# Performance work log

Hardware: AMD Instinct MI355X
Metric: run time of the kernel (lower is better)

## Reference

```python
import jax, jax.numpy as jnp
import numpy as np
from jax import lax

C = 128; HEADS = 16; HD = 8; EPS = 1e-5

def _conv3x3(x, w):
    return lax.conv_general_dilated(x, w, (1, 1), 'SAME', dimension_numbers=('NCHW', 'OIHW', 'NCHW'))

def _cbr3(x, w, g, b):
    # Conv3x3 + BatchNorm(eval, running stats folded -> per-channel affine) + ReLU
    return jax.nn.relu(_conv3x3(x, w) * g[:, None, None] + b[:, None, None])

def _cbr1(x, w, g, b):
    y = jnp.einsum('bchw,oc->bohw', x, w)
    return jax.nn.relu(y * g[:, None, None] + b[:, None, None])

def _ln(t, g, b):
    mu = t.mean(-1, keepdims=True)
    va = ((t - mu) ** 2).mean(-1, keepdims=True)
    return (t - mu) / jnp.sqrt(va + EPS) * g + b

def _gconv1x1(xf, w, b, groups):
    # grouped 1x1 conv on flattened spatial dim: xf [B,Cin,N], w [Cout, Cin//groups]
    B, Cin, N = xf.shape
    Cout = w.shape[0]
    y = jnp.einsum('bgcn,goc->bgon', xf.reshape(B, groups, Cin // groups, N),
                   w.reshape(groups, Cout // groups, Cin // groups))
    return y.reshape(B, Cout, N) + b[:, None]

def _ss_softmax(a):
    # sign * sqrt(|a| + 1e-5) then softmax (GISSA's custom transform)
    a = jnp.sign(a) * jnp.sqrt(jnp.abs(a) + 1e-5)
    return jax.nn.softmax(a, axis=-1)

def _gissa(ximg, qkv_w, qkv_b, g, b, qkv2_w, qkv2_b):
    B, Cc, H, W = ximg.shape
    N = H * W
    xf = ximg.reshape(B, Cc, N)
    qkv = _gconv1x1(xf, qkv_w, qkv_b, HEADS).reshape(B, 3, HEADS, HD, N)
    q, k, v = qkv[:, 0], qkv[:, 1], qkv[:, 2]
    attn = _ss_softmax(jnp.einsum('bhdn,bhen->bhde', q, k) * HD ** -0.5)  # [B,h,hd,hd]
    x1 = jnp.einsum('bhde,bhen->bhdn', attn, v).reshape(B, Cc, N) + xf
    x1 = x1.reshape(B, HEADS, HD, N).transpose(0, 2, 1, 3).reshape(B, Cc, N)  # channel shuffle
    y = x1 * g[:, None] + b[:, None]  # BatchNorm eval affine
    xr = jax.nn.relu(y)
    qkv2 = _gconv1x1(xr, qkv2_w, qkv2_b, HD).reshape(B, 3, HD, HEADS, N)
    q2, k2, v2 = qkv2[:, 0], qkv2[:, 1], qkv2[:, 2]
    attn2 = _ss_softmax(jnp.einsum('bdhn,bdgn->bdhg', q2, k2) * HEADS ** -0.5)  # [B,hd,h,h]
    o = jnp.einsum('bdhg,bdgn->bdhn', attn2, v2).transpose(0, 2, 1, 3).reshape(B, Cc, N) + y
    return o.reshape(B, Cc, H, W)

def _swsa_calc(ximg, pi_w, pi_b, g, b, po_w, po_b):
    B, Cc, H, W = ximg.shape
    t = jnp.einsum('bcn,oc->bon', ximg.reshape(B, Cc, H * W), pi_w) + pi_b[:, None]
    t = t * g[:, None] + b[:, None]  # BN affine
    q = t[:, :Cc].transpose(0, 2, 1)  # [B,N,C]
    v = t[:, Cc:].transpose(0, 2, 1)
    atn = jax.nn.softmax(jnp.einsum('bnc,bmc->bnm', q, q) * Cc ** -0.5, axis=-1)
    y = jnp.einsum('bnm,bmc->bnc', atn, v).transpose(0, 2, 1)  # [B,C,N]
    y = (jnp.einsum('bcn,oc->bon', y, po_w) + po_b[:, None]).reshape(B, Cc, H, W)
    return y, atn

def _swsa_reuse(ximg, atn, pi_w, pi_b, g, b, po_w, po_b):
    B, Cc, H, W = ximg.shape
    t = jnp.einsum('bcn,oc->bon', ximg.reshape(B, Cc, H * W), pi_w) + pi_b[:, None]
    t = t * g[:, None] + b[:, None]
    v = t.transpose(0, 2, 1)
    y = (jnp.einsum('bnm,bmc->bnc', atn, v) * Cc ** -0.5).transpose(0, 2, 1)
    return (jnp.einsum('bcn,oc->bon', y, po_w) + po_b[:, None]).reshape(B, Cc, H, W)

def _forward(x, ssfe_w, ssfe_g, ssfe_b, cc_w, cc_g, cc_b, ln1_g, ln1_b, qkv_w, qkv_b, gbn_g, gbn_b, qkv2_w, qkv2_b, ln2_g, ln2_b, mlp_w1, mlp_b1, mlp_w2, mlp_b2, cs_w, cs_g, cs_b, lfe0_w, lfe0_g, lfe0_b, s0_pi_w, s0_pi_b, s0_bn_g, s0_bn_b, s0_po_w, s0_po_b, lfe1_w, lfe1_g, lfe1_b, s1_pi_w, s1_pi_b, s1_bn_g, s1_bn_b, s1_po_w, s1_po_b, lamuda, fc_w):
    B, Cin, H, W = x.shape
    N = H * W
    # SSFE stem (approximated as Conv3x3+BN+ReLU; source def unavailable)
    xs = _cbr3(x, ssfe_w, ssfe_g, ssfe_b)
    # channel branch: 1x1 CBR + SIT (LN -> GISSA -> residual -> LN -> MLP -> residual)
    xc = _cbr1(xs, cc_w, cc_g, cc_b)
    t = xc.reshape(B, C, N).transpose(0, 2, 1)  # [B,N,C]
    cur = _ln(t, ln1_g, ln1_b).transpose(0, 2, 1).reshape(B, C, H, W)
    t = t + _gissa(cur, qkv_w, qkv_b, gbn_g, gbn_b, qkv2_w, qkv2_b).reshape(B, C, N).transpose(0, 2, 1)
    h = _ln(t, ln2_g, ln2_b)
    h = jax.nn.gelu(h @ mlp_w1.T + mlp_b1, approximate=False) @ mlp_w2.T + mlp_b2
    t = t + h
    xc = t.transpose(0, 2, 1).reshape(B, C, H, W)
    # spatial branch: 3x3 CBR + SCA (LFE + SWSA with attention reuse)
    xp = _cbr3(xs, cs_w, cs_g, cs_b)
    xp = _cbr3(xp, lfe0_w, lfe0_g, lfe0_b) + xp
    y, atn = _swsa_calc(xp, s0_pi_w, s0_pi_b, s0_bn_g, s0_bn_b, s0_po_w, s0_po_b)
    xp = y + xp
    xp = _cbr3(xp, lfe1_w, lfe1_g, lfe1_b) + xp
    xp = _swsa_reuse(xp, atn, s1_pi_w, s1_pi_b, s1_bn_g, s1_bn_b, s1_po_w, s1_po_b) + xp
    lmd = jax.nn.sigmoid(lamuda[0])
    out = lmd * xc + (1.0 - lmd) * xp
    return out.mean(axis=(2, 3)) @ fc_w.T  # global avg pool + fc (dropout p=0 for HUST2013)

def setup_inputs():
    ks = iter(jax.random.split(jax.random.key(0), 64))
    def rn(shape, scale=0.05):
        return jax.random.normal(next(ks), shape, jnp.float32) * scale
    ones = lambda *s: jnp.ones(s, jnp.float32)
    zeros = lambda *s: jnp.zeros(s, jnp.float32)
    return dict(
        x=jax.random.normal(next(ks), (32, 144, 32, 32), jnp.float32),
        ssfe_w=rn((144, 144, 3, 3)), ssfe_g=ones(144), ssfe_b=zeros(144),
        cc_w=rn((128, 144)), cc_g=ones(128), cc_b=zeros(128),
        ln1_g=ones(128), ln1_b=zeros(128),
        qkv_w=rn((384, 8)), qkv_b=zeros(384),
        gbn_g=ones(128), gbn_b=zeros(128),
        qkv2_w=rn((384, 16)), qkv2_b=zeros(384),
        ln2_g=ones(128), ln2_b=zeros(128),
        mlp_w1=rn((512, 128)), mlp_b1=zeros(512),
        mlp_w2=rn((128, 512)), mlp_b2=zeros(128),
        cs_w=rn((128, 144, 3, 3)), cs_g=ones(128), cs_b=zeros(128),
        lfe0_w=rn((128, 128, 3, 3)), lfe0_g=ones(128), lfe0_b=zeros(128),
        s0_pi_w=rn((256, 128)), s0_pi_b=zeros(256), s0_bn_g=ones(256), s0_bn_b=zeros(256),
        s0_po_w=rn((128, 128)), s0_po_b=zeros(128),
        lfe1_w=rn((128, 128, 3, 3)), lfe1_g=ones(128), lfe1_b=zeros(128),
        s1_pi_w=rn((128, 128)), s1_pi_b=zeros(128), s1_bn_g=ones(128), s1_bn_b=zeros(128),
        s1_po_w=rn((128, 128)), s1_po_b=zeros(128),
        lamuda=jnp.full((1,), 0.5, jnp.float32),
        fc_w=rn((16, 128)),
    )

def reference(x, ssfe_w, ssfe_g, ssfe_b, cc_w, cc_g, cc_b, ln1_g, ln1_b, qkv_w, qkv_b, gbn_g, gbn_b, qkv2_w, qkv2_b, ln2_g, ln2_b, mlp_w1, mlp_b1, mlp_w2, mlp_b2, cs_w, cs_g, cs_b, lfe0_w, lfe0_g, lfe0_b, s0_pi_w, s0_pi_b, s0_bn_g, s0_bn_b, s0_po_w, s0_po_b, lfe1_w, lfe1_g, lfe1_b, s1_pi_w, s1_pi_b, s1_bn_g, s1_bn_b, s1_po_w, s1_po_b, lamuda, fc_w):
    return _forward(x, ssfe_w, ssfe_g, ssfe_b, cc_w, cc_g, cc_b, ln1_g, ln1_b, qkv_w, qkv_b, gbn_g, gbn_b, qkv2_w, qkv2_b, ln2_g, ln2_b, mlp_w1, mlp_b1, mlp_w2, mlp_b2, cs_w, cs_g, cs_b, lfe0_w, lfe0_g, lfe0_b, s0_pi_w, s0_pi_b, s0_bn_g, s0_bn_b, s0_po_w, s0_po_b, lfe1_w, lfe1_g, lfe1_b, s1_pi_w, s1_pi_b, s1_bn_g, s1_bn_b, s1_po_w, s1_po_b, lamuda, fc_w)
```

## Files before the change

### kernel.cpp

```cpp
#include <hip/hip_runtime.h>
#include <math.h>


static constexpr int NPIX = 1024;

typedef __attribute__((ext_vector_type(8))) short bf16x8;
typedef __attribute__((ext_vector_type(4))) float f32x4;
typedef __attribute__((ext_vector_type(8))) unsigned short u16x8;
typedef __attribute__((ext_vector_type(4))) unsigned short u16x4;

static __device__ __forceinline__ unsigned short f2bf(float f) {
    unsigned u = __builtin_bit_cast(unsigned, f);
    unsigned r = (u + 0x7fffu + ((u >> 16) & 1u)) >> 16;
    return (unsigned short)r;
}
static __device__ __forceinline__ float bf2f(unsigned short u) {
    unsigned v = ((unsigned)u) << 16;
    return __builtin_bit_cast(float, v);
}

__global__ __launch_bounds__(256) void prepack_convs(
    const float* __restrict__ ssfe_w, const float* __restrict__ cs_w,
    const float* __restrict__ lfe0_w, const float* __restrict__ lfe1_w,
    unsigned short* __restrict__ wssfe, unsigned short* __restrict__ wcs,
    unsigned short* __restrict__ wlfe0, unsigned short* __restrict__ wlfe1)
{
    int idx = blockIdx.x * 256 + threadIdx.x;
    const float* src;
    unsigned short* dst;
    int k, Cout, CIN, CINP;
    if (idx < 207360) {
        src = ssfe_w; dst = wssfe; k = idx; Cout = 144; CIN = 144; CINP = 160;
    } else if (idx < 391680) {
        src = cs_w; dst = wcs; k = idx - 207360; Cout = 128; CIN = 144; CINP = 160;
    } else if (idx < 539136) {
        src = lfe0_w; dst = wlfe0; k = idx - 391680; Cout = 128; CIN = 128; CINP = 128;
    } else if (idx < 686592) {
        src = lfe1_w; dst = wlfe1; k = idx - 539136; Cout = 128; CIN = 128; CINP = 128;
    } else return;
    int ci = k % CINP;
    int rem = k / CINP;
    int co = rem % Cout;
    int tap = rem / Cout;
    float v = (ci < CIN) ? src[((size_t)co * CIN + ci) * 9 + tap] : 0.f;
    dst[k] = f2bf(v);
}

__global__ __launch_bounds__(256) void prepack_lins(
    const float* __restrict__ cc_w, const float* __restrict__ pi0_w,
    const float* __restrict__ pi1_w, const float* __restrict__ po0_w,
    const float* __restrict__ po1_w, const float* __restrict__ w1,
    const float* __restrict__ w2, unsigned short* __restrict__ o)
{
    int idx = blockIdx.x * 256 + threadIdx.x;
    if (idx >= 233472) return;
    float v;
    if (idx < 20480) {
        int ci = idx % 160, co = idx / 160;
        v = (ci < 144) ? cc_w[co * 144 + ci] : 0.f;
    } else if (idx < 53248) {
        v = pi0_w[idx - 20480];
    } else if (idx < 69632) {
        v = pi1_w[idx - 53248];
    } else if (idx < 86016) {
        v = po0_w[idx - 69632];
    } else if (idx < 102400) {
        v = po1_w[idx - 86016];
    } else if (idx < 167936) {
        v = w1[idx - 102400];
    } else {
        v = w2[idx - 167936];
    }
    o[idx] = f2bf(v);
}

template <int CINP, int NCH, int M>
__global__ __launch_bounds__(256) void conv3x3_stg_kernel(
    const float* __restrict__ in, int CIN,
    const unsigned short* __restrict__ wrep,
    const float* __restrict__ g, const float* __restrict__ bb,
    unsigned short* __restrict__ outT, int Cout, int zcol)
{
    __shared__ unsigned short X[194 * 40];
    const int tid = threadIdx.x;
    const int b = blockIdx.x, gr = blockIdx.y, cg = blockIdx.z;
    const int co0 = cg * (M * 16);
    const int pbase = gr << 7;
    const int gbase = pbase - 33;
    const int wv = tid >> 6, lane = tid & 63;
    const int ll = lane & 15, lk = lane >> 4;
    const float* inb = in + ((size_t)b * CIN << 10);

    f32x4 acc[M][2];
#pragma unroll
    for (int i = 0; i < M; ++i)
#pragma unroll
        for (int j = 0; j < 2; ++j)
#pragma unroll
            for (int r = 0; r < 4; ++r) acc[i][j][r] = 0.f;

#pragma unroll 1
    for (int ch = 0; ch < NCH; ++ch) {
        const int c0 = ch << 5;
#pragma unroll 1
        for (int idx = tid; idx < 16 * 194; idx += 256) {
            const int ci2 = idx / 194;
            const int sp = idx - ci2 * 194;
            const int ci = c0 + ci2 * 2;
            const int gp = gbase + sp;
            const bool inr = (gp >= 0) & (gp < 1024);
            const float* p0 = inb + ((size_t)ci << 10);
            float a = (inr && ci < CIN) ? p0[gp] : 0.f;
            float c = (inr && (ci + 1) < CIN) ? p0[gp + 1024] : 0.f;
            *(unsigned*)&X[sp * 40 + ci2 * 2] =
                (unsigned)f2bf(a) | ((unsigned)f2bf(c) << 16);
        }
        __syncthreads();
#pragma unroll
        for (int tap = 0; tap < 9; ++tap) {
            const int soff = (tap / 3) * 32 + (tap % 3);
            const int dx = tap % 3;
            bf16x8 bfrag[2];
#pragma unroll
            for (int j = 0; j < 2; ++j) {
                const int p = wv * 32 + j * 16 + ll;
                bf16x8 v = *(const bf16x8*)&X[(p + soff) * 40 + lk * 8];
                const bool zed = (dx == 0 && j == 0 && ll == 0) ||
                                 (dx == 2 && j == 1 && ll == 15);
                if (zed) { bf16x8 z = {}; v = z; }
                bfrag[j] = v;
            }
            const unsigned short* wb =
                wrep + ((size_t)tap * Cout + co0) * CINP + c0 + lk * 8;
#pragma unroll
            for (int i = 0; i < M; ++i) {
                bf16x8 afr = *(const bf16x8*)(wb + (size_t)(i * 16 + ll) * CINP);
#pragma unroll
                for (int j = 0; j < 2; ++j)
                    acc[i][j] = __builtin_amdgcn_mfma_f32_16x16x32_bf16(
                        afr, bfrag[j], acc[i][j], 0, 0, 0);
            }
        }
        __syncthreads();
    }

#pragma unroll
    for (int i = 0; i < M; ++i) {
#pragma unroll
        for (int j = 0; j < 2; ++j) {
            const int px = pbase + wv * 32 + j * 16 + ll;
            u16x4 tp;
#pragma unroll
            for (int r = 0; r < 4; ++r) {
                const int co = co0 + i * 16 + lk * 4 + r;
                float v = fmaxf(acc[i][j][r] * g[co] + bb[co], 0.f);
                tp[r] = f2bf(v);
            }
            *(u16x4*)(outT + (((size_t)b << 10) + px) * CINP + co0 + i * 16 + lk * 4) = tp;
            if (cg == (int)gridDim.z - 1 && i == 0) {
                u16x4 z = {};
                *(u16x4*)(outT + (((size_t)b << 10) + px) * CINP + zcol + lk * 4) = z;
            }
        }
    }
}

template <int CINP>
__global__ __launch_bounds__(256) void conv3x3_lds_kernel(
    const unsigned short* __restrict__ xT,
    const unsigned short* __restrict__ wrep,
    const float* __restrict__ g, const float* __restrict__ bb,
    const unsigned short* __restrict__ resT,
    unsigned short* __restrict__ outT, int Cout)
{
    constexpr int PITCH = CINP + 8;
    constexpr int NCHK = CINP / 8;
    __shared__ unsigned short X[130 * PITCH];
    const int tid = threadIdx.x;
    const int b = blockIdx.x, gr = blockIdx.y;
    const int pbase = gr << 6;
    const int gbase = pbase - 33;
    const int wid = tid >> 6, lane = tid & 63;
    const int ll = lane & 15, lq = lane >> 4;
    const int co0w = wid << 5;
    const unsigned short* xb = xT + ((size_t)b << 10) * CINP;

#pragma unroll 1
    for (int idx = tid; idx < 130 * NCHK; idx += 256) {
        const int row = idx / NCHK;
        const int chunk = idx - row * NCHK;
        const int gp = gbase + row;
        u16x8 v = {};
        if (gp >= 0 && gp < 1024)
            v = *(const u16x8*)(xb + (size_t)gp * CINP + chunk * 8);
        *(u16x8*)&X[row * PITCH + chunk * 8] = v;
    }
    __syncthreads();

    f32x4 acc[2][4];
#pragma unroll
    for (int i = 0; i < 2; ++i)
#pragma unroll
        for (int j = 0; j < 4; ++j)
#pragma unroll
            for (int r = 0; r < 4; ++r) acc[i][j][r] = 0.f;

#pragma unroll
    for (int tap = 0; tap < 9; ++tap) {
        const int soff = (tap / 3) * 32 + (tap % 3);
        const int dx = tap % 3;
#pragma unroll
        for (int kc = 0; kc < CINP / 32; ++kc) {
            bf16x8 bfv[4];
#pragma unroll
            for (int j = 0; j < 4; ++j) {
                const int p = j * 16 + ll;
                bf16x8 v = *(const bf16x8*)&X[(p + soff) * PITCH + kc * 32 + lq * 8];
                const bool zed = (dx == 0 && (j & 1) == 0 && ll == 0) ||
                                 (dx == 2 && (j & 1) == 1 && ll == 15);
                if (zed) { bf16x8 z = {}; v = z; }
                bfv[j] = v;
            }
            const unsigned short* wb =
                wrep + ((size_t)tap * Cout + co0w) * CINP + kc * 32 + lq * 8;
#pragma unroll
            for (int i = 0; i < 2; ++i) {
                bf16x8 af = *(const bf16x8*)(wb + (size_t)(i * 16 + ll) * CINP);
#pragma unroll
                for (int j = 0; j < 4; ++j)
                    acc[i][j] = __builtin_amdgcn_mfma_f32_16x16x32_bf16(
                        af, bfv[j], acc[i][j], 0, 0, 0);
            }
        }
    }

#pragma unroll
    for (int i = 0; i < 2; ++i) {
        const int cob = co0w + i * 16 + lq * 4;
        float gv[4], bv[4];
#pragma unroll
        for (int r = 0; r < 4; ++r) { gv[r] = g[cob + r]; bv[r] = bb[cob + r]; }
#pragma unroll
        for (int j = 0; j < 4; ++j) {
            const int px = pbase + j * 16 + ll;
            const size_t rowT = ((size_t)((b << 10) + px)) << 7;
            u16x4 rv = {};
            if (resT) rv = *(const u16x4*)(resT + rowT + cob);
            u16x4 tp;
#pragma unroll
            for (int r = 0; r < 4; ++r) {
                float v = fmaxf(acc[i][j][r] * gv[r] + bv[r], 0.f);
                if (resT) v += bf2f(rv[r]);
                tp[r] = f2bf(v);
            }
            *(u16x4*)(outT + rowT + cob) = tp;
        }
    }
}

template <int KP>
__global__ __launch_bounds__(256) void lin_mfma_kernel(
    const unsigned short* __restrict__ xT, const unsigned short* __restrict__ wbf,
    const float* __restrict__ bias0, const float* __restrict__ g,
    const float* __restrict__ bb, const unsigned short* __restrict__ resT,
    float* __restrict__ outF, unsigned short* __restrict__ outBF,
    unsigned short* __restrict__ outT, int do_relu)
{
    const int tid = threadIdx.x;
    const int b = blockIdx.x;
    const int n0 = blockIdx.y << 6;
    const int wid = tid >> 6, lane = tid & 63;
    const int ll = lane & 15, lq = lane >> 4;
    const unsigned short* xb = xT + (size_t)((b << 10) + n0) * KP;

    f32x4 acc[2][4];
#pragma unroll
    for (int i = 0; i < 2; ++i)
#pragma unroll
        for (int j = 0; j < 4; ++j)
#pragma unroll
            for (int r = 0; r < 4; ++r) acc[i][j][r] = 0.f;

#pragma unroll
    for (int kk = 0; kk < KP / 32; ++kk) {
        bf16x8 af[2], bfv[4];
#pragma unroll
        for (int i = 0; i < 2; ++i)
            af[i] = *(const bf16x8*)(wbf + (size_t)(wid * 32 + i * 16 + ll) * KP + kk * 32 + lq * 8);
#pragma unroll
        for (int j = 0; j < 4; ++j)
            bfv[j] = *(const bf16x8*)(xb + (size_t)(j * 16 + ll) * KP + kk * 32 + lq * 8);
#pragma unroll
        for (int i = 0; i < 2; ++i)
#pragma unroll
            for (int j = 0; j < 4; ++j)
                acc[i][j] = __builtin_amdgcn_mfma_f32_16x16x32_bf16(af[i], bfv[j], acc[i][j], 0, 0, 0);
    }

#pragma unroll
    for (int i = 0; i < 2; ++i) {
        const int cob = wid * 32 + i * 16 + lq * 4;
        float b0v[4], gv[4], bv[4];
#pragma unroll
        for (int r = 0; r < 4; ++r) {
            b0v[r] = bias0 ? bias0[cob + r] : 0.f;
            gv[r] = g ? g[cob + r] : 1.f;
            bv[r] = g ? bb[cob + r] : 0.f;
        }
#pragma unroll
        for (int j = 0; j < 4; ++j) {
            const int px = n0 + j * 16 + ll;
            const size_t rowT = ((size_t)((b << 10) + px)) << 7;
            u16x4 rv = {};
            if (resT) rv = *(const u16x4*)(resT + rowT + cob);
            u16x4 tp;
#pragma unroll
            for (int r = 0; r < 4; ++r) {
                const int co = cob + r;
                float v = acc[i][j][r] + b0v[r];
                v = v * gv[r] + bv[r];
                if (do_relu) v = fmaxf(v, 0.f);
                if (resT) v += bf2f(rv[r]);
                if (outF) outF[((size_t)((b << 7) + co) << 10) + px] = v;
                unsigned short h = f2bf(v);
                if (outBF) outBF[((size_t)((b << 7) + co) << 10) + px] = h;
                tp[r] = h;
            }
            if (outT) *(u16x4*)(outT + rowT + cob) = tp;
        }
    }
}

__global__ __launch_bounds__(256) void ln_kernel(
    const float* __restrict__ in, const float* __restrict__ g,
    const float* __restrict__ bb, unsigned short* __restrict__ out_bf,
    unsigned short* __restrict__ outT)
{
    const int tid = threadIdx.x;
    const int b = blockIdx.x >> 2;
    const int n = ((blockIdx.x & 3) << 8) + tid;
    const float* ib = in + ((size_t)b << 17) + n;
    float s = 0.f, sq = 0.f;
#pragma unroll 8
    for (int c = 0; c < 128; ++c) {
        float v = ib[(size_t)c << 10];
        s += v;
        sq += v * v;
    }
    const float mu = s * 0.0078125f;
    const float r = rsqrtf(sq * 0.0078125f - mu * mu + 1e-5f);
    unsigned short* obf = out_bf + ((size_t)b << 17) + n;
    unsigned short* oT = outT + (((size_t)b << 10) + n) * 128;
#pragma unroll 2
    for (int c0 = 0; c0 < 128; c0 += 8) {
        u16x8 pk;
#pragma unroll
        for (int e = 0; e < 8; ++e) {
            const int c = c0 + e;
            float v = ib[(size_t)c << 10];
            float y = (v - mu) * r * g[c] + bb[c];
            unsigned short h = f2bf(y);
            obf[(size_t)c << 10] = h;
            pk[e] = h;
        }
        *(u16x8*)(oT + c0) = pk;
    }
}

__global__ __launch_bounds__(256) void gram_kernel(
    const unsigned short* __restrict__ Xbf, float* __restrict__ G)
{
    __shared__ unsigned short Xs[128 * 128];
    const int tid = threadIdx.x;
    const int b = blockIdx.x >> 2;
    const int rg = blockIdx.x & 3;
    const int wid = tid >> 6, lane = tid & 63;
    const int lq = lane >> 4, ll = lane & 15;
    const unsigned short* Xb = Xbf + ((size_t)b << 17);

    f32x4 acc[2][2];
#pragma unroll
    for (int mi = 0; mi < 2; ++mi)
#pragma unroll
        for (int ci = 0; ci < 2; ++ci)
#pragma unroll
            for (int r = 0; r < 4; ++r) acc[mi][ci][r] = 0.f;

#pragma unroll 1
    for (int nt = 0; nt < 8; ++nt) {
        const int n0 = nt << 7;
#pragma unroll
        for (int p = 0; p < 8; ++p) {
            const int ch = (p << 4) + (tid >> 4);
            const int seg = (tid & 15) << 3;
            *(u16x8*)&Xs[ch * 128 + (seg ^ ((ch & 7) << 3))] =
                *(const u16x8*)(Xb + ((size_t)ch << 10) + n0 + seg);
        }
        __syncthreads();
#pragma unroll
        for (int ks = 0; ks < 4; ++ks) {
            bf16x8 af[2], bf_[2];
#pragma unroll
            for (int mi = 0; mi < 2; ++mi) {
                const int ar = (rg << 5) + mi * 16 + ll;
                af[mi] = *(const bf16x8*)&Xs[ar * 128 + ((ks * 32 + lq * 8) ^ ((ar & 7) << 3))];
            }
#pragma unroll
            for (int ci = 0; ci < 2; ++ci) {
                const int br = (wid << 5) + ci * 16 + ll;
                bf_[ci] = *(const bf16x8*)&Xs[br * 128 + ((ks * 32 + lq * 8) ^ ((br & 7) << 3))];
            }
#pragma unroll
            for (int mi = 0; mi < 2; ++mi)
#pragma unroll
                for (int ci = 0; ci < 2; ++ci)
                    acc[mi][ci] = __builtin_amdgcn_mfma_f32_16x16x32_bf16(
                        af[mi], bf_[ci], acc[mi][ci], 0, 0, 0);
        }
        __syncthreads();
    }
    float* Gb = G + ((size_t)b << 14);
#pragma unroll
    for (int mi = 0; mi < 2; ++mi)
#pragma unroll
        for (int ci = 0; ci < 2; ++ci)
#pragma unroll
            for (int r = 0; r < 4; ++r) {
                const int row = (rg << 5) + mi * 16 + lq * 4 + r;
                const int col = (wid << 5) + ci * 16 + ll;
                Gb[row * 128 + col] = acc[mi][ci][r];
            }
}

__global__ __launch_bounds__(256) void sums_kernel(
    const unsigned short* __restrict__ Xbf, float* __restrict__ S)
{
    const int tid = threadIdx.x;
    const int b = blockIdx.x;
    const int ch = tid >> 1, half = tid & 1;
    const unsigned short* p = Xbf + ((size_t)b << 17) + ((size_t)ch << 10) + half * 512;
    float s = 0.f;
#pragma unroll 4
    for (int i = 0; i < 64; ++i) {
        u16x8 v = *(const u16x8*)(p + i * 8);
#pragma unroll
        for (int e = 0; e < 8; ++e) s += bf2f(v[e]);
    }
    s += __shfl_xor(s, 1);
    if (half == 0) S[(b << 7) + ch] = s;
}

__global__ __launch_bounds__(64) void mats1_kernel(
    const float* __restrict__ G, const float* __restrict__ S,
    const float* __restrict__ qkv_w, const float* __restrict__ qkv_b,
    const float* __restrict__ g, const float* __restrict__ bb,
    unsigned short* __restrict__ M1, float* __restrict__ c1)
{
    const int lane = threadIdx.x;
    const int b = blockIdx.x >> 4, h = blockIdx.x & 15;
    const float* Gb = G + ((size_t)b << 14);
    const float* Sb = S + (b << 7);
    const int d = lane >> 3, e = lane & 7;
    const int qch = h * 8 + d, kch = 128 + h * 8 + e;
    const int qoff = (qch / 24) * 8, koff = (kch / 24) * 8;
    float wq[8], wk[8];
#pragma unroll
    for (int i = 0; i < 8; ++i) {
        wq[i] = qkv_w[qch * 8 + i];
        wk[i] = qkv_w[kch * 8 + i];
    }
    float s = 0.f;
#pragma unroll
    for (int i = 0; i < 8; ++i) {
        float gu = 0.f;
#pragma unroll
        for (int j = 0; j < 8; ++j) gu += Gb[(qoff + i) * 128 + koff + j] * wk[j];
        s += wq[i] * gu;
    }
    const float bq = qkv_b[qch], bk = qkv_b[kch];
    float swk = 0.f, swq = 0.f;
#pragma unroll
    for (int j = 0; j < 8; ++j) { swk += wk[j] * Sb[koff + j]; swq += wq[j] * Sb[qoff + j]; }
    s += bq * swk + bk * swq + 1024.f * bq * bk;
    s *= 0.35355339059327373f;
    float a = (s > 0.f) ? sqrtf(s + 1e-5f) : ((s < 0.f) ? -sqrtf(1e-5f - s) : 0.f);
    float mx = a;
    mx = fmaxf(mx, __shfl_xor(mx, 1));
    mx = fmaxf(mx, __shfl_xor(mx, 2));
    mx = fmaxf(mx, __shfl_xor(mx, 4));
    float p = __expf(a - mx);
    float den = p;
    den += __shfl_xor(den, 1);
    den += __shfl_xor(den, 2);
    den += __shfl_xor(den, 4);
    const float A = p / den;

    const int l = e;
    const int cp = d * 16 + h;
    float row[16];
#pragma unroll
    for (int j = 0; j < 16; ++j) row[j] = 0.f;
    float cacc = 0.f;
#pragma unroll
    for (int e2 = 0; e2 < 8; ++e2) {
        const float Ae = __shfl(A, d * 8 + e2);
        const int vch = 256 + h * 8 + e2;
        const int voff = (vch / 24) * 8;
        cacc += Ae * qkv_b[vch];
        if ((voff >> 4) == l) {
            const int base = voff & 15;
#pragma unroll
            for (int j = 0; j < 8; ++j) row[base + j] += Ae * qkv_w[vch * 8 + j];
        }
    }
    const int idc = h * 8 + d;
    if ((idc >> 4) == l) row[idc & 15] += 1.f;
    const float gg = g[cp];
    unsigned short* mrow = M1 + ((size_t)b << 14) + cp * 128 + l * 16;
#pragma unroll
    for (int j = 0; j < 16; ++j) mrow[j] = f2bf(gg * row[j]);
    if (l == 0) c1[(b << 7) + cp] = gg * cacc + bb[cp];
}

__global__ __launch_bounds__(256) void mats2_kernel(
    const float* __restrict__ G, const float* __restrict__ S,
    const float* __restrict__ qkv2_w, const float* __restrict__ qkv2_b,
    unsigned short* __restrict__ M2, float* __restrict__ c2)
{
    const int tid = threadIdx.x;
    const int b = blockIdx.x >> 3, d = blockIdx.x & 7;
    const float* Gb = G + ((size_t)b << 14);
    const float* Sb = S + (b << 7);
    const int h = tid >> 4, gq = tid & 15;
    const int q2ch = d * 16 + h, k2ch = 128 + d * 16 + gq;
    const int qoff = (q2ch / 48) * 16, koff = (k2ch / 48) * 16;
    float wq[16], wk[16];
#pragma unroll
    for (int i = 0; i < 16; ++i) {
        wq[i] = qkv2_w[q2ch * 16 + i];
        wk[i] = qkv2_w[k2ch * 16 + i];
    }
    float s = 0.f;
#pragma unroll
    for (int i = 0; i < 16; ++i) {
        float gu = 0.f;
#pragma unroll
        for (int j = 0; j < 16; ++j) gu += Gb[(qoff + i) * 128 + koff + j] * wk[j];
        s += wq[i] * gu;
    }
    const float bq = qkv2_b[q2ch], bk = qkv2_b[k2ch];
    float swk = 0.f, swq = 0.f;
#pragma unroll
    for (int j = 0; j < 16; ++j) { swk += wk[j] * Sb[koff + j]; swq += wq[j] * Sb[qoff + j]; }
    s += bq * swk + bk * swq + 1024.f * bq * bk;
    s *= 0.25f;
    float a = (s > 0.f) ? sqrtf(s + 1e-5f) : ((s < 0.f) ? -sqrtf(1e-5f - s) : 0.f);
    float mx = a;
    mx = fmaxf(mx, __shfl_xor(mx, 1));
    mx = fmaxf(mx, __shfl_xor(mx, 2));
    mx = fmaxf(mx, __shfl_xor(mx, 4));
    mx = fmaxf(mx, __shfl_xor(mx, 8));
    float p = __expf(a - mx);
    float den = p;
    den += __shfl_xor(den, 1);
    den += __shfl_xor(den, 2);
    den += __shfl_xor(den, 4);
    den += __shfl_xor(den, 8);
    const float A2 = p / den;

    const int l = gq;
    float row[8];
#pragma unroll
    for (int j = 0; j < 8; ++j) row[j] = 0.f;
    float cacc = 0.f;
#pragma unroll
    for (int g2 = 0; g2 < 16; ++g2) {
        const float Ag = __shfl(A2, (tid & 48) + g2);
        const int v2ch = 256 + d * 16 + g2;
        const int voff = (v2ch / 48) * 16;
        cacc += Ag * qkv2_b[v2ch];
        if ((l >> 1) == (voff >> 4)) {
            const int base = (l & 1) * 8;
#pragma unroll
            for (int j = 0; j < 8; ++j) row[j] += Ag * qkv2_w[v2ch * 16 + base + j];
        }
    }
    const int c = h * 8 + d;
    unsigned short* mrow = M2 + ((size_t)b << 14) + c * 128 + l * 8;
#pragma unroll
    for (int j = 0; j < 8; ++j) mrow[j] = f2bf(row[j]);
    if (l == 0) c2[(b << 7) + c] = cacc;
}

__global__ __launch_bounds__(256) void apply1_mfma_kernel(
    const unsigned short* __restrict__ curT, const unsigned short* __restrict__ M1bf,
    const float* __restrict__ c1, float* __restrict__ ybuf,
    unsigned short* __restrict__ yrbf, unsigned short* __restrict__ yrT)
{
    const int tid = threadIdx.x;
    const int b = blockIdx.x >> 3;
    const int n0 = (blockIdx.x & 7) << 7;
    const int wid = tid >> 6, lane = tid & 63;
    const int wr = wid >> 1, wc = wid & 1;
    const int ll = lane & 15, lq = lane >> 4;
    const unsigned short* Mb = M1bf + ((size_t)b << 14);
    const unsigned short* xb = curT + (((size_t)b << 10) + n0 + wc * 64) * 128;

    f32x4 acc[4][4];
#pragma unroll
    for (int i = 0; i < 4; ++i)
#pragma unroll
        for (int j = 0; j < 4; ++j)
#pragma unroll
            for (int r = 0; r < 4; ++r) acc[i][j][r] = 0.f;

#pragma unroll
    for (int kk = 0; kk < 4; ++kk) {
        bf16x8 af[4], bfv[4];
#pragma unroll
        for (int i = 0; i < 4; ++i)
            af[i] = *(const bf16x8*)(Mb + (size_t)(wr * 64 + i * 16 + ll) * 128 + kk * 32 + lq * 8);
#pragma unroll
        for (int j = 0; j < 4; ++j)
            bfv[j] = *(const bf16x8*)(xb + (size_t)(j * 16 + ll) * 128 + kk * 32 + lq * 8);
#pragma unroll
        for (int i = 0; i < 4; ++i)
#pragma unroll
            for (int j = 0; j < 4; ++j)
                acc[i][j] = __builtin_amdgcn_mfma_f32_16x16x32_bf16(af[i], bfv[j], acc[i][j], 0, 0, 0);
    }

#pragma unroll
    for (int i = 0; i < 4; ++i) {
        const int cob = wr * 64 + i * 16 + lq * 4;
        float c1v[4];
#pragma unroll
        for (int r = 0; r < 4; ++r) c1v[r] = c1[(b << 7) + cob + r];
#pragma unroll
        for (int j = 0; j < 4; ++j) {
            const int px = n0 + wc * 64 + j * 16 + ll;
            u16x4 tp;
#pragma unroll
            for (int r = 0; r < 4; ++r) {
                const int co = cob + r;
                const float v = acc[i][j][r] + c1v[r];
                const size_t oi = ((size_t)(b * 128 + co) << 10) + px;
                ybuf[oi] = v;
                const unsigned short h = f2bf(fmaxf(v, 0.f));
                yrbf[oi] = h;
                tp[r] = h;
            }
            *(u16x4*)(yrT + (((size_t)b << 10) + px) * 128 + cob) = tp;
        }
    }
}

__global__ __launch_bounds__(256) void apply2_mfma_kernel(
    const unsigned short* __restrict__ yrT, const unsigned short* __restrict__ M2bf,
    const float* __restrict__ c2, const float* __restrict__ ybuf,
    float* __restrict__ t)
{
    const int tid = threadIdx.x;
    const int b = blockIdx.x >> 3;
    const int n0 = (blockIdx.x & 7) << 7;
    const int wid = tid >> 6, lane = tid & 63;
    const int wr = wid >> 1, wc = wid & 1;
    const int ll = lane & 15, lq = lane >> 4;
    const unsigned short* Mb = M2bf + ((size_t)b << 14);
    const unsigned short* xb = yrT + (((size_t)b << 10) + n0 + wc * 64) * 128;

    f32x4 acc[4][4];
#pragma unroll
    for (int i = 0; i < 4; ++i)
#pragma unroll
        for (int j = 0; j < 4; ++j)
#pragma unroll
            for (int r = 0; r < 4; ++r) acc[i][j][r] = 0.f;

#pragma unroll
    for (int kk = 0; kk < 4; ++kk) {
        bf16x8 af[4], bfv[4];
#pragma unroll
        for (int i = 0; i < 4; ++i)
            af[i] = *(const bf16x8*)(Mb + (size_t)(wr * 64 + i * 16 + ll) * 128 + kk * 32 + lq * 8);
#pragma unroll
        for (int j = 0; j < 4; ++j)
            bfv[j] = *(const bf16x8*)(xb + (size_t)(j * 16 + ll) * 128 + kk * 32 + lq * 8);
#pragma unroll
        for (int i = 0; i < 4; ++i)
#pragma unroll
            for (int j = 0; j < 4; ++j)
                acc[i][j] = __builtin_amdgcn_mfma_f32_16x16x32_bf16(af[i], bfv[j], acc[i][j], 0, 0, 0);
    }

#pragma unroll
    for (int i = 0; i < 4; ++i) {
        const int cob = wr * 64 + i * 16 + lq * 4;
        float c2v[4];
#pragma unroll
        for (int r = 0; r < 4; ++r) c2v[r] = c2[(b << 7) + cob + r];
#pragma unroll
        for (int j = 0; j < 4; ++j) {
            const int px = n0 + wc * 64 + j * 16 + ll;
#pragma unroll
            for (int r = 0; r < 4; ++r) {
                const size_t oi = ((size_t)(b * 128 + cob + r) << 10) + px;
                t[oi] += acc[i][j][r] + c2v[r] + ybuf[oi];
            }
        }
    }
}

__global__ __launch_bounds__(256) void mlp_mfma_kernel(
    float* __restrict__ t, const float* __restrict__ ln_g,
    const float* __restrict__ ln_b, const unsigned short* __restrict__ w1bf,
    const float* __restrict__ b1, const unsigned short* __restrict__ w2bf,
    const float* __restrict__ b2)
{
    __shared__ unsigned char lds[16384 + 65536];
    unsigned char* xnb = lds;
    unsigned char* hb = lds + 16384;

    const int tid = threadIdx.x;
    const int b = blockIdx.x >> 4;
    const int n0 = (blockIdx.x & 15) << 6;
    float* tb = t + ((size_t)b << 17) + n0;

    {
        const int px = tid >> 2, q = tid & 3;
        float v[32];
        float s = 0.f, sq = 0.f;
#pragma unroll
        for (int k = 0; k < 32; ++k) {
            float x = tb[((size_t)(q * 32 + k) << 10) + px];
            v[k] = x;
            s += x;
            sq += x * x;
        }
        s += __shfl_xor(s, 1); s += __shfl_xor(s, 2);
        sq += __shfl_xor(sq, 1); sq += __shfl_xor(sq, 2);
        const float mu = s * 0.0078125f;
        const float rstd = rsqrtf(sq * 0.0078125f - mu * mu + 1e-5f);
        const int sw = (px & 7) << 4;
#pragma unroll
        for (int cc = 0; cc < 4; ++cc) {
            u16x8 pk;
#pragma unroll
            for (int e = 0; e < 8; ++e) {
                int c = q * 32 + cc * 8 + e;
                float xv = (v[cc * 8 + e] - mu) * rstd * ln_g[c] + ln_b[c];
                pk[e] = f2bf(xv);
            }
            *(u16x8*)(xnb + px * 256 + ((q * 64 + cc * 16) ^ sw)) = pk;
        }
    }
    __syncthreads();

    const int wid = tid >> 6, lane = tid & 63;
    const int lr = lane & 15, lk = lane >> 4;

#pragma unroll 1
    for (int pass = 0; pass < 2; ++pass) {
        const int hidbase = (wid << 7) + (pass << 6);
        f32x4 acc[4][4];
#pragma unroll
        for (int i = 0; i < 4; ++i)
#pragma unroll
            for (int j = 0; j < 4; ++j)
#pragma unroll
                for (int r = 0; r < 4; ++r) acc[i][j][r] = 0.f;
#pragma unroll
        for (int kk = 0; kk < 4; ++kk) {
            bf16x8 af[4], bfr[4];
#pragma unroll
            for (int i = 0; i < 4; ++i)
                af[i] = *(const bf16x8*)(w1bf + (size_t)(hidbase + i * 16 + lr) * 128 + kk * 32 + lk * 8);
#pragma unroll
            for (int j = 0; j < 4; ++j) {
                const int px = j * 16 + lr;
                bfr[j] = *(const bf16x8*)(xnb + px * 256 + ((kk * 64 + lk * 16) ^ ((px & 7) << 4)));
            }
#pragma unroll
            for (int i = 0; i < 4; ++i)
#pragma unroll
                for (int j = 0; j < 4; ++j)
                    acc[i][j] = __builtin_amdgcn_mfma_f32_16x16x32_bf16(af[i], bfr[j], acc[i][j], 0, 0, 0);
        }
#pragma unroll
        for (int i = 0; i < 4; ++i) {
            const int hid0 = hidbase + i * 16 + lk * 4;
            float bi[4];
#pragma unroll
            for (int r = 0; r < 4; ++r) bi[r] = b1[hid0 + r];
#pragma unroll
            for (int j = 0; j < 4; ++j) {
                const int px = j * 16 + lr;
                u16x4 pk;
#pragma unroll
                for (int r = 0; r < 4; ++r) {
                    float x = acc[i][j][r] + bi[r];
                    float u = 1.5957691f * x * (1.f + 0.044715f * x * x);
                    float gv = x / (1.f + __expf(-u));
                    pk[r] = f2bf(gv);
                }
                *(u16x4*)(hb + px * 1024 + ((hid0 * 2) ^ ((px & 7) << 4))) = pk;
            }
        }
    }
    __syncthreads();

    f32x4 acc2[2][4];
#pragma unroll
    for (int i = 0; i < 2; ++i)
#pragma unroll
        for (int j = 0; j < 4; ++j)
#pragma unroll
            for (int r = 0; r < 4; ++r) acc2[i][j][r] = 0.f;
#pragma unroll 2
    for (int ks = 0; ks < 16; ++ks) {
        bf16x8 af[2], bfr[4];
#pragma unroll
        for (int i = 0; i < 2; ++i)
            af[i] = *(const bf16x8*)(w2bf + (size_t)((wid << 5) + i * 16 + lr) * 512 + ks * 32 + lk * 8);
#pragma unroll
        for (int j = 0; j < 4; ++j) {
            const int px = j * 16 + lr;
            bfr[j] = *(const bf16x8*)(hb + px * 1024 + ((ks * 64 + lk * 16) ^ ((px & 7) << 4)));
        }
#pragma unroll
        for (int i = 0; i < 2; ++i)
#pragma unroll
            for (int j = 0; j < 4; ++j)
                acc2[i][j] = __builtin_amdgcn_mfma_f32_16x16x32_bf16(af[i], bfr[j], acc2[i][j], 0, 0, 0);
    }
#pragma unroll
    for (int i = 0; i < 2; ++i) {
        const int cb = (wid << 5) + i * 16 + lk * 4;
        float b2v[4];
#pragma unroll
        for (int r = 0; r < 4; ++r) b2v[r] = b2[cb + r];
#pragma unroll
        for (int j = 0; j < 4; ++j) {
            const int px = j * 16 + lr;
#pragma unroll
            for (int r = 0; r < 4; ++r) {
                const size_t off = ((size_t)(cb + r) << 10) + px;
                tb[off] += acc2[i][j][r] + b2v[r];
            }
        }
    }
}

__global__ __launch_bounds__(256) void swsa_mfma_kernel(
    const unsigned short* __restrict__ qT, const unsigned short* __restrict__ vbf,
    float* __restrict__ outp, unsigned short* __restrict__ outT, float fscale)
{
    __shared__ unsigned short K_lds[128 * 128];
    __shared__ unsigned short V_lds[128 * 128];
    const int tid = threadIdx.x;
    const int b = blockIdx.x & 31;
    const int n0 = (blockIdx.x >> 5) << 6;
    const int wid = tid >> 6, lane = tid & 63;
    const int lq = lane >> 4, ll = lane & 15;
    const unsigned short* qTb = qT + ((size_t)b << 17);
    const unsigned short* vb = vbf + ((size_t)b << 17);

    bf16x8 aq[4];
    {
        const int row = n0 + wid * 16 + ll;
#pragma unroll
        for (int kk = 0; kk < 4; ++kk)
            aq[kk] = *(const bf16x8*)(qTb + ((size_t)row << 7) + kk * 32 + lq * 8);
    }

    float mrun[4], lrun[4];
#pragma unroll
    for (int i = 0; i < 4; ++i) { mrun[i] = -INFINITY; lrun[i] = 0.f; }
    f32x4 yacc[8];
#pragma unroll
    for (int cj = 0; cj < 8; ++cj)
#pragma unroll
        for (int r = 0; r < 4; ++r) yacc[cj][r] = 0.f;

#pragma unroll 1
    for (int mt = 0; mt < 8; ++mt) {
        const int m0 = mt << 7;
        for (int ch = tid; ch < 2048; ch += 256) {
            const int rr = ch >> 4, e0 = (ch & 15) << 3;
            const int sw = (rr & 7) << 3;
            *(u16x8*)&K_lds[rr * 128 + (e0 ^ sw)] =
                *(const u16x8*)(qTb + ((size_t)(m0 + rr) << 7) + e0);
            *(u16x8*)&V_lds[rr * 128 + (e0 ^ sw)] =
                *(const u16x8*)(vb + ((size_t)rr << 10) + m0 + e0);
        }
        __syncthreads();

        f32x4 sacc[8];
#pragma unroll
        for (int j = 0; j < 8; ++j)
#pragma unroll
            for (int r = 0; r < 4; ++r) sacc[j][r] = 0.f;
#pragma unroll
        for (int j = 0; j < 8; ++j) {
            const int ml = j * 16 + ll;
            const int swk = (ml & 7) << 3;
#pragma unroll
            for (int kk = 0; kk < 4; ++kk) {
                bf16x8 bk = *(const bf16x8*)&K_lds[ml * 128 + ((kk * 32 + lq * 8) ^ swk)];
                sacc[j] = __builtin_amdgcn_mfma_f32_16x16x32_bf16(aq[kk], bk, sacc[j], 0, 0, 0);
            }
        }
        __syncthreads();

        float pmax[4];
#pragma unroll
        for (int i = 0; i < 4; ++i) pmax[i] = -INFINITY;
#pragma unroll
        for (int j = 0; j < 8; ++j)
#pragma unroll
            for (int r = 0; r < 4; ++r) {
                float s = sacc[j][r] * 0.08838834764831845f;
                sacc[j][r] = s;
                pmax[r] = fmaxf(pmax[r], s);
            }
        float alpha[4];
#pragma unroll
        for (int i = 0; i < 4; ++i) {
            float m = pmax[i];
            m = fmaxf(m, __shfl_xor(m, 1));
            m = fmaxf(m, __shfl_xor(m, 2));
            m = fmaxf(m, __shfl_xor(m, 4));
            m = fmaxf(m, __shfl_xor(m, 8));
            const float mn = fmaxf(mrun[i], m);
            alpha[i] = __expf(mrun[i] - mn);
            mrun[i] = mn;
        }
        float psum[4];
#pragma unroll
        for (int r = 0; r < 4; ++r) {
            const int nbw = wid * 16 + lq * 4 + r;
            const int sw4 = ((nbw >> 2) & 3) << 4;
            const float mn = mrun[r];
            float ps = 0.f;
#pragma unroll
            for (int j = 0; j < 8; ++j) {
                float p = __expf(sacc[j][r] - mn);
                ps += p;
                K_lds[nbw * 128 + ((j * 16 + ll) ^ sw4)] = f2bf(p);
            }
            psum[r] = ps;
        }
#pragma unroll
        for (int i = 0; i < 4; ++i) {
            float s = psum[i];
            s += __shfl_xor(s, 1);
            s += __shfl_xor(s, 2);
            s += __shfl_xor(s, 4);
            s += __shfl_xor(s, 8);
            lrun[i] = lrun[i] * alpha[i] + s;
        }
#pragma unroll
        for (int cj = 0; cj < 8; ++cj)
#pragma unroll
            for (int r = 0; r < 4; ++r) yacc[cj][r] *= alpha[r];

        bf16x8 ap[4];
        {
            const int nb = wid * 16 + ll;
            const int sw4 = ((nb >> 2) & 3) << 4;
#pragma unroll
            for (int mk = 0; mk < 4; ++mk)
                ap[mk] = *(const bf16x8*)&K_lds[nb * 128 + ((mk * 32 + lq * 8) ^ sw4)];
        }
#pragma unroll
        for (int cj = 0; cj < 8; ++cj) {
            const int cl = cj * 16 + ll;
            const int sw = (cl & 7) << 3;
#pragma unroll
            for (int mk = 0; mk < 4; ++mk) {
                bf16x8 bv = *(const bf16x8*)&V_lds[cl * 128 + ((mk * 32 + lq * 8) ^ sw)];
                yacc[cj] = __builtin_amdgcn_mfma_f32_16x16x32_bf16(ap[mk], bv, yacc[cj], 0, 0, 0);
            }
        }
        __syncthreads();
    }

    const int nbase = n0 + wid * 16 + lq * 4;
    float inv[4];
#pragma unroll
    for (int r = 0; r < 4; ++r) inv[r] = fscale / lrun[r];
#pragma unroll
    for (int cj = 0; cj < 8; ++cj) {
        const int c = cj * 16 + ll;
        float4 o;
        o.x = yacc[cj][0] * inv[0];
        o.y = yacc[cj][1] * inv[1];
        o.z = yacc[cj][2] * inv[2];
        o.w = yacc[cj][3] * inv[3];
        if (outp)
            *(float4*)(outp + ((size_t)(b * 128 + c) << 10) + nbase) = o;
        if (outT) {
            unsigned short* tb = outT + ((size_t)((b << 10) + nbase)) * 128 + c;
            tb[0] = f2bf(o.x);
            tb[128] = f2bf(o.y);
            tb[256] = f2bf(o.z);
            tb[384] = f2bf(o.w);
        }
    }
}

__global__ __launch_bounds__(256) void mean_kernel(
    const float* __restrict__ xc, const float* __restrict__ xp,
    const float* __restrict__ lamuda, float* __restrict__ meanb)
{
    const int wid = threadIdx.x >> 6, lane = threadIdx.x & 63;
    const int row = (blockIdx.x << 2) + wid;
    const float lmd = 1.f / (1.f + __expf(-lamuda[0]));
    const float* a = xc + ((size_t)row << 10) + (lane << 2);
    const float* d = xp + ((size_t)row << 10) + (lane << 2);
    float s = 0.f;
#pragma unroll
    for (int i = 0; i < 4; ++i) {
        float4 va = *(const float4*)(a + (i << 8));
        float4 vd = *(const float4*)(d + (i << 8));
        s += lmd * (va.x + va.y + va.z + va.w) +
             (1.f - lmd) * (vd.x + vd.y + vd.z + vd.w);
    }
#pragma unroll
    for (int o = 1; o < 64; o <<= 1) s += __shfl_xor(s, o);
    if (lane == 0) meanb[row] = s * (1.f / 1024.f);
}

__global__ __launch_bounds__(256) void fc_kernel(
    const float* __restrict__ meanb, const float* __restrict__ fc_w,
    float* __restrict__ outp)
{
    const int idx = blockIdx.x * 256 + threadIdx.x;
    if (idx >= 512) return;
    const int b = idx >> 4, o = idx & 15;
    float s = 0.f;
#pragma unroll 4
    for (int c = 0; c < 128; ++c) s += fc_w[o * 128 + c] * meanb[b * 128 + c];
    outp[b * 16 + o] = s;
}

extern "C" void kernel_launch(void* const* d_in, const int* in_sizes, int n_in,
                              void* d_out, int out_size, void* d_ws, size_t ws_size,
                              hipStream_t stream)
{
    (void)in_sizes; (void)n_in; (void)out_size; (void)ws_size;

    const float* x       = (const float*)d_in[0];
    const float* ssfe_w  = (const float*)d_in[1];
    const float* ssfe_g  = (const float*)d_in[2];
    const float* ssfe_b  = (const float*)d_in[3];
    const float* cc_w    = (const float*)d_in[4];
    const float* cc_g    = (const float*)d_in[5];
    const float* cc_b    = (const float*)d_in[6];
    const float* ln1_g   = (const float*)d_in[7];
    const float* ln1_b   = (const float*)d_in[8];
    const float* qkv_w   = (const float*)d_in[9];
    const float* qkv_b   = (const float*)d_in[10];
    const float* gbn_g   = (const float*)d_in[11];
    const float* gbn_b   = (const float*)d_in[12];
    const float* qkv2_w  = (const float*)d_in[13];
    const float* qkv2_b  = (const float*)d_in[14];
    const float* ln2_g   = (const float*)d_in[15];
    const float* ln2_b   = (const float*)d_in[16];
    const float* mlp_w1  = (const float*)d_in[17];
    const float* mlp_b1  = (const float*)d_in[18];
    const float* mlp_w2  = (const float*)d_in[19];
    const float* mlp_b2  = (const float*)d_in[20];
    const float* cs_w    = (const float*)d_in[21];
    const float* cs_g    = (const float*)d_in[22];
    const float* cs_b    = (const float*)d_in[23];
    const float* lfe0_w  = (const float*)d_in[24];
    const float* lfe0_g  = (const float*)d_in[25];
    const float* lfe0_b  = (const float*)d_in[26];
    const float* s0_pi_w = (const float*)d_in[27];
    const float* s0_pi_b = (const float*)d_in[28];
    const float* s0_bn_g = (const float*)d_in[29];
    const float* s0_bn_b = (const float*)d_in[30];
    const float* s0_po_w = (const float*)d_in[31];
    const float* s0_po_b = (const float*)d_in[32];
    const float* lfe1_w  = (const float*)d_in[33];
    const float* lfe1_g  = (const float*)d_in[34];
    const float* lfe1_b  = (const float*)d_in[35];
    const float* s1_pi_w = (const float*)d_in[36];
    const float* s1_pi_b = (const float*)d_in[37];
    const float* s1_bn_g = (const float*)d_in[38];
    const float* s1_bn_b = (const float*)d_in[39];
    const float* s1_po_w = (const float*)d_in[40];
    const float* s1_po_b = (const float*)d_in[41];
    const float* lamuda  = (const float*)d_in[42];
    const float* fc_w    = (const float*)d_in[43];
    float* out = (float*)d_out;
    float* ws = (float*)d_ws;

    float* xs = ws;
    float* t  = ws + 4718592;
    float* P1 = ws + 8912896;
    float* Qr = ws + 13107200;
    float* P2 = ws + 25690112;
    float* P3 = ws + 29884416;

    unsigned short* curbf = (unsigned short*)Qr;
    unsigned short* curT  = (unsigned short*)(Qr + 2097152);
    unsigned short* yrbf  = (unsigned short*)(Qr + 4194304);
    unsigned short* yrT   = (unsigned short*)(Qr + 6291456);
    unsigned short* xsT   = (unsigned short*)(Qr + 8388608);
    float* ybuf = P2;

    unsigned short* xpT   = (unsigned short*)Qr;
    unsigned short* qT0   = (unsigned short*)Qr;
    unsigned short* v0    = (unsigned short*)(Qr + 2097152);
    unsigned short* yvT   = (unsigned short*)(Qr + 4194304);
    unsigned short* v1    = (unsigned short*)(Qr + 4194304);
    unsigned short* xp3T  = (unsigned short*)(Qr + 6291456);
    unsigned short* yv2T  = (unsigned short*)(Qr + 6291456);
    unsigned short* xp2T  = (unsigned short*)(Qr + 8388608);
    unsigned short* xp4T  = (unsigned short*)(Qr + 8388608);

    unsigned short* linw  = (unsigned short*)(Qr + 11010048);
    unsigned short* wcc   = linw;
    unsigned short* wpi0  = linw + 20480;
    unsigned short* wpi1  = linw + 53248;
    unsigned short* wpo0  = linw + 69632;
    unsigned short* wpo1  = linw + 86016;
    unsigned short* w1bf  = linw + 102400;
    unsigned short* w2bf  = linw + 167936;
    float* meanb = Qr + 11200000;

    float* Gbuf  = P3 + 1048576;
    float* Sbuf  = P3 + 1572864;
    unsigned short* M1bf = (unsigned short*)(P3 + 1576960);
    float* c1buf = P3 + 1839104;
    unsigned short* M2bf = (unsigned short*)(P3 + 1843200);
    float* c2buf = P3 + 2105344;

    unsigned short* wssfe = (unsigned short*)P3;
    unsigned short* wcs   = (unsigned short*)(P3 + 131072);
    unsigned short* wlfe0 = (unsigned short*)(P3 + 262144);
    unsigned short* wlfe1 = (unsigned short*)xs;

    const dim3 blk(256);

    prepack_convs<<<dim3((686592 + 255) / 256), blk, 0, stream>>>(
        ssfe_w, cs_w, lfe0_w, lfe1_w, wssfe, wcs, wlfe0, wlfe1);
    prepack_lins<<<dim3((233472 + 255) / 256), blk, 0, stream>>>(
        cc_w, s0_pi_w, s1_pi_w, s0_po_w, s1_po_w, mlp_w1, mlp_w2, linw);

    conv3x3_stg_kernel<160, 5, 3><<<dim3(32, 8, 3), blk, 0, stream>>>(
        x, 144, wssfe, ssfe_g, ssfe_b, xsT, 144, 144);
    lin_mfma_kernel<160><<<dim3(32, 16), blk, 0, stream>>>(
        xsT, wcc, nullptr, cc_g, cc_b, nullptr, t, nullptr, nullptr, 1);

    ln_kernel<<<dim3(128), blk, 0, stream>>>(t, ln1_g, ln1_b, curbf, curT);
    gram_kernel<<<dim3(128), blk, 0, stream>>>(curbf, Gbuf);
    sums_kernel<<<dim3(32), blk, 0, stream>>>(curbf, Sbuf);
    mats1_kernel<<<dim3(512), dim3(64), 0, stream>>>(Gbuf, Sbuf, qkv_w, qkv_b, gbn_g, gbn_b, M1bf, c1buf);
    apply1_mfma_kernel<<<dim3(256), blk, 0, stream>>>(curT, M1bf, c1buf, ybuf, yrbf, yrT);
    gram_kernel<<<dim3(128), blk, 0, stream>>>(yrbf, Gbuf);
    sums_kernel<<<dim3(32), blk, 0, stream>>>(yrbf, Sbuf);
    mats2_kernel<<<dim3(256), blk, 0, stream>>>(Gbuf, Sbuf, qkv2_w, qkv2_b, M2bf, c2buf);
    apply2_mfma_kernel<<<dim3(256), blk, 0, stream>>>(yrT, M2bf, c2buf, ybuf, t);

    mlp_mfma_kernel<<<dim3(512), blk, 0, stream>>>(t, ln2_g, ln2_b, w1bf, mlp_b1, w2bf, mlp_b2);

    conv3x3_lds_kernel<160><<<dim3(32, 16), blk, 0, stream>>>(
        xsT, wcs, cs_g, cs_b, nullptr, xpT, 128);
    conv3x3_lds_kernel<128><<<dim3(32, 16), blk, 0, stream>>>(
        xpT, wlfe0, lfe0_g, lfe0_b, xpT, xp2T, 128);
    lin_mfma_kernel<128><<<dim3(32, 16), blk, 0, stream>>>(
        xp2T, wpi0, s0_pi_b, s0_bn_g, s0_bn_b, nullptr, nullptr, nullptr, qT0, 0);
    lin_mfma_kernel<128><<<dim3(32, 16), blk, 0, stream>>>(
        xp2T, wpi0 + (size_t)128 * 128, s0_pi_b + 128, s0_bn_g + 128, s0_bn_b + 128,
        nullptr, nullptr, v0, nullptr, 0);
    swsa_mfma_kernel<<<dim3(512), blk, 0, stream>>>(qT0, v0, nullptr, yvT, 1.0f);
    lin_mfma_kernel<128><<<dim3(32, 16), blk, 0, stream>>>(
        yvT, wpo0, s0_po_b, nullptr, nullptr, xp2T, nullptr, nullptr, xp3T, 0);
    conv3x3_lds_kernel<128><<<dim3(32, 16), blk, 0, stream>>>(
        xp3T, wlfe1, lfe1_g, lfe1_b, xp3T, xp4T, 128);
    lin_mfma_kernel<128><<<dim3(32, 16), blk, 0, stream>>>(
        xp4T, wpi1, s1_pi_b, s1_bn_g, s1_bn_b, nullptr, nullptr, v1, nullptr, 0);
    swsa_mfma_kernel<<<dim3(512), blk, 0, stream>>>(qT0, v1, nullptr, yv2T, 0.08838834764831845f);
    lin_mfma_kernel<128><<<dim3(32, 16), blk, 0, stream>>>(
        yv2T, wpo1, s1_po_b, nullptr, nullptr, xp4T, P3, nullptr, nullptr, 0);

    mean_kernel<<<dim3(1024), blk, 0, stream>>>(t, P3, lamuda, meanb);
    fc_kernel<<<dim3(2), blk, 0, stream>>>(meanb, fc_w, out);
}
```

Baseline: 457.4 us.

## Pre-transpose input to bf16 pixel-major and restructure first conv3x3 tiling

Adds a separate kernel that converts the fp32 NCHW input into a bf16 pixel-major layout padded to 160 channels. The first 3x3 conv then loads the whole 130-row halo once into LDS with vectorized 16-byte loads, instead of converting strided fp32 per channel chunk. Each block now covers 64 pixels and all 144 output channels, with three waves each computing 48 channels and the fourth wave only zeroing the pad columns. This removes the redundant input re-reads and conversions across the three output-channel groups, at the cost of an extra kernel launch and an intermediate buffer round trip. It also leaves one wave idle during the MFMA work.

```diff
diff --git a/kernel.cpp b/kernel.cpp
--- a/kernel.cpp
+++ b/kernel.cpp
@@ -74,93 +74,129 @@
     o[idx] = f2bf(v);
 }
 
-template <int CINP, int NCH, int M>
-__global__ __launch_bounds__(256) void conv3x3_stg_kernel(
-    const float* __restrict__ in, int CIN,
+__global__ __launch_bounds__(256) void cvt_xT_kernel(
+    const float* __restrict__ x, unsigned short* __restrict__ xT0)
+{
+    __shared__ unsigned short T[64 * 168];
+    const int tid = threadIdx.x;
+    const int b = blockIdx.x;
+    const int px0 = blockIdx.y << 6;
+    const float* xb = x + ((size_t)b * 144 << 10) + px0;
+
+#pragma unroll 1
+    for (int idx = tid; idx < 72 * 64; idx += 256) {
+        const int c2 = idx >> 6, px = idx & 63;
+        float a = xb[((size_t)(2 * c2) << 10) + px];
+        float c = xb[((size_t)(2 * c2 + 1) << 10) + px];
+        *(unsigned*)&T[px * 168 + 2 * c2] =
+            (unsigned)f2bf(a) | ((unsigned)f2bf(c) << 16);
+    }
+#pragma unroll 1
+    for (int idx = tid; idx < 64 * 8; idx += 256) {
+        const int px = idx >> 3, pr = idx & 7;
+        *(unsigned*)&T[px * 168 + 144 + pr * 2] = 0u;
+    }
+    __syncthreads();
+
+#pragma unroll 1
+    for (int idx = tid; idx < 64 * 20; idx += 256) {
+        const int px = idx / 20;
+        const int chunk = idx - px * 20;
+        *(u16x8*)(xT0 + ((size_t)((b << 10) + px0 + px)) * 160 + chunk * 8) =
+            *(const u16x8*)&T[px * 168 + chunk * 8];
+    }
+}
+
+__global__ __launch_bounds__(256) void conv3x3_ssfe_kernel(
+    const unsigned short* __restrict__ xT,
     const unsigned short* __restrict__ wrep,
     const float* __restrict__ g, const float* __restrict__ bb,
-    unsigned short* __restrict__ outT, int Cout, int zcol)
-{
-    __shared__ unsigned short X[194 * 40];
+    unsigned short* __restrict__ outT)
+{
+    constexpr int CINP = 160, PITCH = 168, NCHK = 20;
+    __shared__ unsigned short X[130 * PITCH];
     const int tid = threadIdx.x;
-    const int b = blockIdx.x, gr = blockIdx.y, cg = blockIdx.z;
-    const int co0 = cg * (M * 16);
-    const int pbase = gr << 7;
+    const int b = blockIdx.x, gr = blockIdx.y;
+    const int pbase = gr << 6;
     const int gbase = pbase - 33;
-    const int wv = tid >> 6, lane = tid & 63;
-    const int ll = lane & 15, lk = lane >> 4;
-    const float* inb = in + ((size_t)b * CIN << 10);
-
-    f32x4 acc[M][2];
-#pragma unroll
-    for (int i = 0; i < M; ++i)
-#pragma unroll
-        for (int j = 0; j < 2; ++j)
+    const int wid = tid >> 6, lane = tid & 63;
+    const int ll = lane & 15, lq = lane >> 4;
+    const unsigned short* xb = xT + ((size_t)b << 10) * CINP;
+
+#pragma unroll 1
+    for (int idx = tid; idx < 130 * NCHK; idx += 256) {
+        const int row = idx / NCHK;
+        const int chunk = idx - row * NCHK;
+        const int gp = gbase + row;
+        u16x8 v = {};
+        if (gp >= 0 && gp < 1024)
+            v = *(const u16x8*)(xb + (size_t)gp * CINP + chunk * 8);
+        *(u16x8*)&X[row * PITCH + chunk * 8] = v;
+    }
+    __syncthreads();
+
+    if (wid == 3) {
+#pragma unroll
+        for (int j = 0; j < 4; ++j) {
+            const int px = pbase + j * 16 + ll;
+            u16x4 z = {};
+            *(u16x4*)(outT + ((size_t)((b << 10) + px)) * 160 + 144 + lq * 4) = z;
+        }
+        return;
+    }
+
+    const int co0w = wid * 48;
+    f32x4 acc[3][4];
+#pragma unroll
+    for (int i = 0; i < 3; ++i)
+#pragma unroll
+        for (int j = 0; j < 4; ++j)
 #pragma unroll
             for (int r = 0; r < 4; ++r) acc[i][j][r] = 0.f;
 
-#pragma unroll 1
-    for (int ch = 0; ch < NCH; ++ch) {
-        const int c0 = ch << 5;
-#pragma unroll 1
-        for (int idx = tid; idx < 16 * 194; idx += 256) {
-            const int ci2 = idx / 194;
-            const int sp = idx - ci2 * 194;
-            const int ci = c0 + ci2 * 2;
-            const int gp = gbase + sp;
-            const bool inr = (gp >= 0) & (gp < 1024);
-            const float* p0 = inb + ((size_t)ci << 10);
-            float a = (inr && ci < CIN) ? p0[gp] : 0.f;
-            float c = (inr && (ci + 1) < CIN) ? p0[gp + 1024] : 0.f;
-            *(unsigned*)&X[sp * 40 + ci2 * 2] =
-                (unsigned)f2bf(a) | ((unsigned)f2bf(c) << 16);
-        }
-        __syncthreads();
-#pragma unroll
-        for (int tap = 0; tap < 9; ++tap) {
-            const int soff = (tap / 3) * 32 + (tap % 3);
-            const int dx = tap % 3;
-            bf16x8 bfrag[2];
-#pragma unroll
-            for (int j = 0; j < 2; ++j) {
-                const int p = wv * 32 + j * 16 + ll;
-                bf16x8 v = *(const bf16x8*)&X[(p + soff) * 40 + lk * 8];
-                const bool zed = (dx == 0 && j == 0 && ll == 0) ||
-                                 (dx == 2 && j == 1 && ll == 15);
+#pragma unroll
+    for (int tap = 0; tap < 9; ++tap) {
+        const int soff = (tap / 3) * 32 + (tap % 3);
+        const int dx = tap % 3;
+#pragma unroll
+        for (int kc = 0; kc < CINP / 32; ++kc) {
+            bf16x8 bfv[4];
+#pragma unroll
+            for (int j = 0; j < 4; ++j) {
+                const int p = j * 16 + ll;
+                bf16x8 v = *(const bf16x8*)&X[(p + soff) * PITCH + kc * 32 + lq * 8];
+                const bool zed = (dx == 0 && (j & 1) == 0 && ll == 0) ||
+                                 (dx == 2 && (j & 1) == 1 && ll == 15);
                 if (zed) { bf16x8 z = {}; v = z; }
-                bfrag[j] = v;
+                bfv[j] = v;
             }
             const unsigned short* wb =
-                wrep + ((size_t)tap * Cout + co0) * CINP + c0 + lk * 8;
-#pragma unroll
-            for (int i = 0; i < M; ++i) {
-                bf16x8 afr = *(const bf16x8*)(wb + (size_t)(i * 16 + ll) * CINP);
-#pragma unroll
-                for (int j = 0; j < 2; ++j)
+                wrep + ((size_t)tap * 144 + co0w) * CINP + kc * 32 + lq * 8;
+#pragma unroll
+            for (int i = 0; i < 3; ++i) {
+                bf16x8 af = *(const bf16x8*)(wb + (size_t)(i * 16 + ll) * CINP);
+#pragma unroll
+                for (int j = 0; j < 4; ++j)
                     acc[i][j] = __builtin_amdgcn_mfma_f32_16x16x32_bf16(
-                        afr, bfrag[j], acc[i][j], 0, 0, 0);
-            }
-        }
-        __syncthreads();
-    }
-
-#pragma unroll
-    for (int i = 0; i < M; ++i) {
-#pragma unroll
-        for (int j = 0; j < 2; ++j) {
-            const int px = pbase + wv * 32 + j * 16 + ll;
+                        af, bfv[j], acc[i][j], 0, 0, 0);
+            }
+        }
+    }
+
+#pragma unroll
+    for (int i = 0; i < 3; ++i) {
+        const int cob = co0w + i * 16 + lq * 4;
+        float gv[4], bv[4];
+#pragma unroll
+        for (int r = 0; r < 4; ++r) { gv[r] = g[cob + r]; bv[r] = bb[cob + r]; }
+#pragma unroll
+        for (int j = 0; j < 4; ++j) {
+            const int px = pbase + j * 16 + ll;
             u16x4 tp;
 #pragma unroll
-            for (int r = 0; r < 4; ++r) {
-                const int co = co0 + i * 16 + lk * 4 + r;
-                float v = fmaxf(acc[i][j][r] * g[co] + bb[co], 0.f);
-                tp[r] = f2bf(v);
-            }
-            *(u16x4*)(outT + (((size_t)b << 10) + px) * CINP + co0 + i * 16 + lk * 4) = tp;
-            if (cg == (int)gridDim.z - 1 && i == 0) {
-                u16x4 z = {};
-                *(u16x4*)(outT + (((size_t)b << 10) + px) * CINP + zcol + lk * 4) = z;
-            }
+            for (int r = 0; r < 4; ++r)
+                tp[r] = f2bf(fmaxf(acc[i][j][r] * gv[r] + bv[r], 0.f));
+            *(u16x4*)(outT + ((size_t)((b << 10) + px)) * 160 + cob) = tp;
         }
     }
 }
@@ -1103,6 +1139,9 @@
     float* Qr = ws + 13107200;
     float* P2 = ws + 25690112;
     float* P3 = ws + 29884416;
+    (void)P1;
+
+    unsigned short* xT0 = (unsigned short*)Qr;
 
     unsigned short* curbf = (unsigned short*)Qr;
     unsigned short* curT  = (unsigned short*)(Qr + 2097152);
@@ -1150,8 +1189,9 @@
     prepack_lins<<<dim3((233472 + 255) / 256), blk, 0, stream>>>(
         cc_w, s0_pi_w, s1_pi_w, s0_po_w, s1_po_w, mlp_w1, mlp_w2, linw);
 
-    conv3x3_stg_kernel<160, 5, 3><<<dim3(32, 8, 3), blk, 0, stream>>>(
-        x, 144, wssfe, ssfe_g, ssfe_b, xsT, 144, 144);
+    cvt_xT_kernel<<<dim3(32, 16), blk, 0, stream>>>(x, xT0);
+    conv3x3_ssfe_kernel<<<dim3(32, 16), blk, 0, stream>>>(
+        xT0, wssfe, ssfe_g, ssfe_b, xsT);
     lin_mfma_kernel<160><<<dim3(32, 16), blk, 0, stream>>>(
         xsT, wcc, nullptr, cc_g, cc_b, nullptr, t, nullptr, nullptr, 1);
 
```

New measurement: 449.4 us. No clear change (-1.7%).
